# Optimization experiments

Measured on AMD Instinct MI355X. Metric: run time of the kernel, lower is better.

Reference implementation:

```python
import jax, jax.numpy as jnp
import numpy as np

HEAD_DIM = 256
NUM_HEADS = 8
NUM_KV_HEADS = 1
ROPE_BASE = 10000.0
NEG_INF = -1e9


def _rope_cos_sin(position_ids):
    # inv_freq: [head_dim/2]
    inv_freq = 1.0 / (ROPE_BASE ** (jnp.arange(0, HEAD_DIM, 2, dtype=jnp.float32) / HEAD_DIM))
    # freqs: [B, S, head_dim/2]
    freqs = position_ids.astype(jnp.float32)[:, :, None] * inv_freq[None, None, :]
    emb = jnp.concatenate([freqs, freqs], axis=-1)  # [B, S, head_dim]
    return jnp.cos(emb), jnp.sin(emb)


def _rotate_half(x):
    x1, x2 = x[..., : HEAD_DIM // 2], x[..., HEAD_DIM // 2 :]
    return jnp.concatenate([-x2, x1], axis=-1)


def setup_inputs() -> dict:
    key = jax.random.key(0)
    ks = jax.random.split(key, 5)
    B, S, D = 2, 2048, 2048
    hidden_states = jax.random.normal(ks[0], (B, S, D), dtype=jnp.float32)
    # additive causal mask: 0 on/below diagonal, -1e9 above
    causal = jnp.triu(jnp.full((S, S), NEG_INF, dtype=jnp.float32), k=1)
    attention_mask = jnp.broadcast_to(causal[None, None], (B, 1, S, S))
    position_ids = jnp.broadcast_to(jnp.arange(S, dtype=jnp.int64 if jax.config.jax_enable_x64 else jnp.int32)[None], (B, S))
    Wq = jax.random.normal(ks[1], (NUM_HEADS * HEAD_DIM, D), dtype=jnp.float32) * 0.02
    Wk = jax.random.normal(ks[2], (NUM_KV_HEADS * HEAD_DIM, D), dtype=jnp.float32) * 0.02
    Wv = jax.random.normal(ks[3], (NUM_KV_HEADS * HEAD_DIM, D), dtype=jnp.float32) * 0.02
    Wo = jax.random.normal(ks[4], (D, NUM_HEADS * HEAD_DIM), dtype=jnp.float32) * 0.02
    return {"hidden_states": hidden_states, "attention_mask": attention_mask,
            "position_ids": position_ids, "Wq": Wq, "Wk": Wk, "Wv": Wv, "Wo": Wo}


def reference(hidden_states, attention_mask, position_ids, Wq, Wk, Wv, Wo):
    B, S, D = hidden_states.shape
    n_rep = NUM_HEADS // NUM_KV_HEADS
    # projections (no bias)
    q = (hidden_states @ Wq.T).reshape(B, S, NUM_HEADS, HEAD_DIM).transpose(0, 2, 1, 3)
    k = (hidden_states @ Wk.T).reshape(B, S, NUM_KV_HEADS, HEAD_DIM).transpose(0, 2, 1, 3)
    v = (hidden_states @ Wv.T).reshape(B, S, NUM_KV_HEADS, HEAD_DIM).transpose(0, 2, 1, 3)
    # rotary embeddings, broadcast over heads (unsqueeze_dim=1)
    cos, sin = _rope_cos_sin(position_ids)  # [B, S, head_dim]
    cos, sin = cos[:, None], sin[:, None]
    q = q * cos + _rotate_half(q) * sin
    k = k * cos + _rotate_half(k) * sin
    # repeat_kv: expand kv heads to match query heads
    k = jnp.repeat(k, n_rep, axis=1)  # [B, H, S, Dh]
    v = jnp.repeat(v, n_rep, axis=1)
    scores = jnp.einsum('bhqd,bhkd->bhqk', q, k) / jnp.sqrt(jnp.float32(HEAD_DIM))
    scores = scores + attention_mask
    attn_weights = jax.nn.softmax(scores.astype(jnp.float32), axis=-1).astype(q.dtype)
    attn_output = jnp.einsum('bhqk,bhkd->bhqd', attn_weights, v)
    attn_output = attn_output.transpose(0, 2, 1, 3).reshape(B, S, NUM_HEADS * HEAD_DIM)
    attn_output = attn_output @ Wo.T
    return attn_output, attn_weights
```

## Files before the change

kernel.cpp:

```cpp
#include <hip/hip_runtime.h>
#include <math.h>

#define SEQ 2048
#define DM  2048
#define NH  8
#define HD  256
#define NB  2

typedef __attribute__((ext_vector_type(8))) short bf16x8;
typedef __attribute__((ext_vector_type(4))) float f32x4;

__device__ inline short f2b(float f) {
    union { float f; unsigned u; } x; x.f = f;
    unsigned r = x.u + 0x7fffu + ((x.u >> 16) & 1u);
    return (short)(r >> 16);
}
__device__ inline float b2f(short s) {
    union { unsigned u; float f; } x;
    x.u = ((unsigned)(unsigned short)s) << 16;
    return x.f;
}

typedef unsigned int u32_g __attribute__((address_space(1)));
typedef unsigned int u32_l __attribute__((address_space(3)));
__device__ inline void gl2lds(const void* g, void* l) {
    __builtin_amdgcn_global_load_lds((const u32_g*)g, (u32_l*)l, 16, 0, 0);
}

__global__ void convert_all(const float* __restrict__ hs, const float* __restrict__ wq,
                            const float* __restrict__ wk, const float* __restrict__ wv,
                            const float* __restrict__ wo,
                            short* __restrict__ hsb, short* __restrict__ wcat,
                            short* __restrict__ wob)
{
    int i4 = blockIdx.x * 256 + threadIdx.x;
    const float* src; short* dst; int s4, d4;
    if (i4 < 2097152)      { src = hs; dst = hsb;  s4 = i4;           d4 = s4; }
    else if (i4 < 3145728) { src = wq; dst = wcat; s4 = i4 - 2097152; d4 = s4; }
    else if (i4 < 3276800) { src = wk; dst = wcat; s4 = i4 - 3145728; d4 = 1048576 + s4; }
    else if (i4 < 3407872) { src = wv; dst = wcat; s4 = i4 - 3276800; d4 = 1179648 + s4; }
    else                   { src = wo; dst = wob;  s4 = i4 - 3407872; d4 = s4; }
    float4 v = ((const float4*)src)[s4];
    short4 o;
    o.x = f2b(v.x); o.y = f2b(v.y); o.z = f2b(v.z); o.w = f2b(v.w);
    ((short4*)dst)[d4] = o;
}

template<int MODE>
__global__ __launch_bounds__(256, 2) void gemm_bt(const short* __restrict__ A,
                                                  const short* __restrict__ Bw,
                                                  float* __restrict__ C,
                                                  short* __restrict__ q_o,
                                                  short* __restrict__ k_o,
                                                  short* __restrict__ v_o,
                                                  int M, int N, int K)
{
    __shared__ short As[128 * 32];
    __shared__ short Bs[128 * 32];
    int tid = threadIdx.x;
    int lane = tid & 63, w = tid >> 6;
    int lm = lane & 15, quad = lane >> 4;
    int wm = w & 1, wn = w >> 1;
    int m0 = blockIdx.y * 128, n0 = blockIdx.x * 128;

    f32x4 acc[16];
#pragma unroll
    for (int i = 0; i < 16; ++i) acc[i] = (f32x4){0.f, 0.f, 0.f, 0.f};

    const char* Aptr = (const char*)A + (size_t)m0 * K * 2;
    const char* Bptr = (const char*)Bw + (size_t)n0 * K * 2;

    for (int k0 = 0; k0 < K; k0 += 32) {
#pragma unroll
        for (int it = 0; it < 2; ++it) {
            int f = it * 4096 + tid * 16;
            int row = f >> 6, colb = f & 63;
            gl2lds(Aptr + (size_t)row * (K * 2) + k0 * 2 + colb, (char*)As + f);
            gl2lds(Bptr + (size_t)row * (K * 2) + k0 * 2 + colb, (char*)Bs + f);
        }
        __syncthreads();
        bf16x8 af[4], bfr[4];
#pragma unroll
        for (int mt = 0; mt < 4; ++mt)
            af[mt] = *(const bf16x8*)(As + (wm * 64 + mt * 16 + lm) * 32 + quad * 8);
#pragma unroll
        for (int nt = 0; nt < 4; ++nt)
            bfr[nt] = *(const bf16x8*)(Bs + (wn * 64 + nt * 16 + lm) * 32 + quad * 8);
#pragma unroll
        for (int mt = 0; mt < 4; ++mt)
#pragma unroll
            for (int nt = 0; nt < 4; ++nt)
                acc[mt * 4 + nt] = __builtin_amdgcn_mfma_f32_16x16x32_bf16(
                    af[mt], bfr[nt], acc[mt * 4 + nt], 0, 0, 0);
        __syncthreads();
    }

#pragma unroll
    for (int mt = 0; mt < 4; ++mt)
#pragma unroll
        for (int nt = 0; nt < 4; ++nt) {
            f32x4 a = acc[mt * 4 + nt];
            int col = n0 + wn * 64 + nt * 16 + lm;
#pragma unroll
            for (int i = 0; i < 4; ++i) {
                int m = m0 + wm * 64 + mt * 16 + quad * 4 + i;
                if (MODE == 0) {
                    C[(size_t)m * N + col] = a[i];
                } else {
                    int b = m >> 11, s = m & (SEQ - 1);
                    short hv = f2b(a[i]);
                    if (col < DM) {
                        int hh = col >> 8, d = col & (HD - 1);
                        q_o[(((size_t)(b * NH + hh)) * SEQ + s) * HD + d] = hv;
                    } else if (col < DM + HD) {
                        int d = col - DM;
                        int c2 = (d >> 3) ^ (s & 31);
                        k_o[((size_t)b * SEQ + s) * HD + (c2 << 3) + (d & 7)] = hv;
                    } else {
                        int d = col - DM - HD;
                        int sc = ((s >> 3) & 7) ^ (d & 7);
                        v_o[((size_t)(b * HD + d)) * SEQ + (s & ~63) + (sc << 3) + (s & 7)] = hv;
                    }
                }
            }
        }
}

__global__ void rope_kernel(short* __restrict__ q, short* __restrict__ k,
                            const int* __restrict__ pos)
{
    const int QP = NB * NH * SEQ * 128;
    const int KP = NB * SEQ * 128;
    const float C0 = 0.07195578415606394f;
    int idx = blockIdx.x * 256 + threadIdx.x;
    if (idx < QP) {
        int d = idx & 127;
        int s = (idx >> 7) & (SEQ - 1);
        int h = (idx >> 18) & (NH - 1);
        int b = idx >> 21;
        float p = (float)pos[b * SEQ + s];
        float fr = p * expf(-(float)d * C0);
        float c = cosf(fr), sn = sinf(fr);
        size_t base = (((size_t)(b * NH + h)) * SEQ + s) * HD + d;
        float x0 = b2f(q[base]), x1 = b2f(q[base + 128]);
        q[base]       = f2b(x0 * c - x1 * sn);
        q[base + 128] = f2b(x1 * c + x0 * sn);
    } else {
        int j = idx - QP;
        if (j < KP) {
            int d = j & 127;
            int s = (j >> 7) & (SEQ - 1);
            int b = j >> 18;
            float p = (float)pos[b * SEQ + s];
            float fr = p * expf(-(float)d * C0);
            float c = cosf(fr), sn = sinf(fr);
            int e0 = ((((d >> 3) ^ (s & 31)) & 31) << 3) | (d & 7);
            size_t base = ((size_t)(b * SEQ + s)) * HD;
            float x0 = b2f(k[base + e0]), x1 = b2f(k[base + (e0 ^ 128)]);
            k[base + e0]         = f2b(x0 * c - x1 * sn);
            k[base + (e0 ^ 128)] = f2b(x1 * c + x0 * sn);
        }
    }
}

__global__ __launch_bounds__(256, 2) void attn_flash(const short* __restrict__ qb,
                                                     const short* __restrict__ kb,
                                                     const short* __restrict__ vT,
                                                     float* __restrict__ w_out,
                                                     short* __restrict__ a_o)
{
    __shared__ short Ks[64 * 256];
    __shared__ short Vs[256 * 64];
    __shared__ short P[4][16][72];

    int tid = threadIdx.x;
    int w = tid >> 6, lane = tid & 63;
    int lm = lane & 15, quad = lane >> 4;
    int idx = blockIdx.x;
    int hb = idx & 15;
    int h = hb & 7, b = hb >> 3;
    int tq = 31 - (idx >> 4);
    int q0 = tq * 64;
    int r0 = q0 + w * 16;

    const short* qrow = qb + (((size_t)(b * NH + h)) * SEQ + r0 + lm) * HD;
    bf16x8 qf[8];
#pragma unroll
    for (int ks = 0; ks < 8; ++ks)
        qf[ks] = *(const bf16x8*)(qrow + ks * 32 + quad * 8);

    float m_r[4], l_r[4];
    f32x4 O[16];
#pragma unroll
    for (int i = 0; i < 4; ++i) { m_r[i] = -INFINITY; l_r[i] = 0.f; }
#pragma unroll
    for (int i = 0; i < 16; ++i) O[i] = (f32x4){0.f, 0.f, 0.f, 0.f};

    const short* kb0 = kb + (size_t)b * SEQ * HD;
    const short* vb0 = vT + (size_t)b * HD * SEQ;

    for (int tk = 0; tk <= tq; ++tk) {
        const char* kt = (const char*)(kb0 + (size_t)tk * 64 * HD);
#pragma unroll
        for (int it = 0; it < 8; ++it) {
            int g = it * 256 + tid;
            gl2lds(kt + ((size_t)(g >> 5) * HD + (g & 31) * 8) * 2, (char*)Ks + g * 16);
            gl2lds((const char*)vb0 + ((size_t)(g >> 3) * SEQ + tk * 64 + (g & 7) * 8) * 2,
                   (char*)Vs + g * 16);
        }
        __syncthreads();

        f32x4 sa[4];
#pragma unroll
        for (int nt = 0; nt < 4; ++nt) sa[nt] = (f32x4){0.f, 0.f, 0.f, 0.f};
#pragma unroll
        for (int ks = 0; ks < 8; ++ks)
#pragma unroll
            for (int nt = 0; nt < 4; ++nt) {
                int s_l = nt * 16 + lm;
                bf16x8 kf = *(const bf16x8*)(Ks + s_l * 256 +
                                             (((ks * 4 + quad) ^ (s_l & 31)) << 3));
                sa[nt] = __builtin_amdgcn_mfma_f32_16x16x32_bf16(qf[ks], kf, sa[nt], 0, 0, 0);
            }

        float vals[4][4];
#pragma unroll
        for (int nt = 0; nt < 4; ++nt)
#pragma unroll
            for (int i = 0; i < 4; ++i) {
                float v = sa[nt][i] * 0.0625f;
                if (tk == tq && (nt * 16 + lm) > (w * 16 + quad * 4 + i)) v -= 1e9f;
                vals[nt][i] = v;
            }
        float mnew[4], alpha[4], ps[4];
#pragma unroll
        for (int i = 0; i < 4; ++i) {
            float mx = fmaxf(fmaxf(vals[0][i], vals[1][i]), fmaxf(vals[2][i], vals[3][i]));
            mx = fmaxf(mx, __shfl_xor(mx, 1));
            mx = fmaxf(mx, __shfl_xor(mx, 2));
            mx = fmaxf(mx, __shfl_xor(mx, 4));
            mx = fmaxf(mx, __shfl_xor(mx, 8));
            mnew[i] = fmaxf(m_r[i], mx);
            alpha[i] = expf(m_r[i] - mnew[i]);
            ps[i] = 0.f;
        }
#pragma unroll
        for (int nt = 0; nt < 4; ++nt)
#pragma unroll
            for (int i = 0; i < 4; ++i) {
                float p = expf(vals[nt][i] - mnew[i]);
                ps[i] += p;
                P[w][quad * 4 + i][nt * 16 + lm] = f2b(p);
            }
        f32x4 al;
#pragma unroll
        for (int i = 0; i < 4; ++i) {
            float t = ps[i];
            t += __shfl_xor(t, 1); t += __shfl_xor(t, 2);
            t += __shfl_xor(t, 4); t += __shfl_xor(t, 8);
            l_r[i] = l_r[i] * alpha[i] + t;
            m_r[i] = mnew[i];
            al[i] = alpha[i];
        }
#pragma unroll
        for (int nt2 = 0; nt2 < 16; ++nt2) O[nt2] *= al;

        const short* prow = &P[w][lm][0];
#pragma unroll
        for (int kc = 0; kc < 2; ++kc) {
            bf16x8 pf = *(const bf16x8*)(prow + kc * 32 + quad * 8);
#pragma unroll
            for (int nt2 = 0; nt2 < 16; ++nt2) {
                int d_l = nt2 * 16 + lm;
                bf16x8 vf = *(const bf16x8*)(Vs + d_l * 64 +
                                             (((kc * 4 + quad) ^ (d_l & 7)) << 3));
                O[nt2] = __builtin_amdgcn_mfma_f32_16x16x32_bf16(pf, vf, O[nt2], 0, 0, 0);
            }
        }
        __syncthreads();
    }

    f32x4 li;
#pragma unroll
    for (int i = 0; i < 4; ++i) li[i] = 1.f / l_r[i];

#pragma unroll
    for (int nt2 = 0; nt2 < 16; ++nt2)
#pragma unroll
        for (int i = 0; i < 4; ++i) {
            size_t s = (size_t)q0 + w * 16 + quad * 4 + i;
            a_o[((size_t)b * SEQ + s) * DM + h * HD + nt2 * 16 + lm] = f2b(O[nt2][i] * li[i]);
        }

    float* wb = w_out + (((size_t)(b * NH + h)) * SEQ) * SEQ;
    for (int tk = 0; tk <= tq; ++tk) {
        const char* kt = (const char*)(kb0 + (size_t)tk * 64 * HD);
#pragma unroll
        for (int it = 0; it < 8; ++it) {
            int g = it * 256 + tid;
            gl2lds(kt + ((size_t)(g >> 5) * HD + (g & 31) * 8) * 2, (char*)Ks + g * 16);
        }
        __syncthreads();
        f32x4 sa[4];
#pragma unroll
        for (int nt = 0; nt < 4; ++nt) sa[nt] = (f32x4){0.f, 0.f, 0.f, 0.f};
#pragma unroll
        for (int ks = 0; ks < 8; ++ks)
#pragma unroll
            for (int nt = 0; nt < 4; ++nt) {
                int s_l = nt * 16 + lm;
                bf16x8 kf = *(const bf16x8*)(Ks + s_l * 256 +
                                             (((ks * 4 + quad) ^ (s_l & 31)) << 3));
                sa[nt] = __builtin_amdgcn_mfma_f32_16x16x32_bf16(qf[ks], kf, sa[nt], 0, 0, 0);
            }
#pragma unroll
        for (int nt = 0; nt < 4; ++nt)
#pragma unroll
            for (int i = 0; i < 4; ++i) {
                float v = sa[nt][i] * 0.0625f;
                if (tk == tq && (nt * 16 + lm) > (w * 16 + quad * 4 + i)) v -= 1e9f;
                float wv = expf(v - m_r[i]) * li[i];
                wb[(size_t)(r0 + quad * 4 + i) * SEQ + tk * 64 + nt * 16 + lm] = wv;
            }
        __syncthreads();
    }

    int zs = (tq + 1) * 64;
    if (zs < SEQ) {
        int r = tid >> 2, c0 = (tid & 3) * 4;
        float* wr = wb + (size_t)(q0 + r) * SEQ;
        float4 z = make_float4(0.f, 0.f, 0.f, 0.f);
        for (int c = zs + c0; c < SEQ; c += 16)
            *(float4*)(wr + c) = z;
    }
}

extern "C" void kernel_launch(void* const* d_in, const int* in_sizes, int n_in,
                              void* d_out, int out_size, void* d_ws, size_t ws_size,
                              hipStream_t stream)
{
    const float* hs   = (const float*)d_in[0];
    const int*   pos  = (const int*)d_in[2];
    const float* Wq   = (const float*)d_in[3];
    const float* Wk   = (const float*)d_in[4];
    const float* Wv   = (const float*)d_in[5];
    const float* Wo   = (const float*)d_in[6];

    float* out      = (float*)d_out;
    float* attn_out = out;
    float* w_out    = out + (size_t)NB * SEQ * DM;

    short* hsb  = (short*)d_ws;
    short* a_b  = hsb;
    short* wcat = hsb + 8388608;
    short* wob  = wcat + 5242880;
    short* qx   = wob + 4194304;
    short* kx   = qx + 8388608;
    short* vTx  = kx + 1048576;

    convert_all<<<17408, 256, 0, stream>>>(hs, Wq, Wk, Wv, Wo, hsb, wcat, wob);
    gemm_bt<1><<<dim3(20, 32), 256, 0, stream>>>(hsb, wcat, nullptr, qx, kx, vTx,
                                                 NB * SEQ, DM + 2 * HD, DM);
    rope_kernel<<<18432, 256, 0, stream>>>(qx, kx, pos);
    attn_flash<<<512, 256, 0, stream>>>(qx, kx, vTx, w_out, a_b);
    gemm_bt<0><<<dim3(16, 32), 256, 0, stream>>>(a_b, wob, attn_out, nullptr, nullptr, nullptr,
                                                 NB * SEQ, DM, DM);
}
```

Baseline: 650.9 us.

## Register-prefetch K/V tiles, fast math exp/trig, nontemporal stores, zigzag tile order

The attention kernel now prefetches the next K/V tile into registers while the current tile is computed, replacing direct global-to-LDS loads with a register-staged double buffer. It also raises wave priority around the MFMA loops, switches expf and sincos to hardware approximations (with explicit range reduction for RoPE), writes the attention weights with nontemporal stores, and alternates the query-tile order between long and short tiles across blocks for load balance. The register staging adds register pressure and may lower occupancy, and the fast math functions lose some accuracy.

```diff
diff --git a/kernel.cpp b/kernel.cpp
--- a/kernel.cpp
+++ b/kernel.cpp
@@ -132,6 +132,7 @@
     const int QP = NB * NH * SEQ * 128;
     const int KP = NB * SEQ * 128;
     const float C0 = 0.07195578415606394f;
+    const float R2PI = 0.15915494309189535f;
     int idx = blockIdx.x * 256 + threadIdx.x;
     if (idx < QP) {
         int d = idx & 127;
@@ -139,8 +140,9 @@
         int h = (idx >> 18) & (NH - 1);
         int b = idx >> 21;
         float p = (float)pos[b * SEQ + s];
-        float fr = p * expf(-(float)d * C0);
-        float c = cosf(fr), sn = sinf(fr);
+        float fr = p * __expf(-(float)d * C0);
+        float rv = fr * R2PI; rv -= floorf(rv);
+        float c = __builtin_amdgcn_cosf(rv), sn = __builtin_amdgcn_sinf(rv);
         size_t base = (((size_t)(b * NH + h)) * SEQ + s) * HD + d;
         float x0 = b2f(q[base]), x1 = b2f(q[base + 128]);
         q[base]       = f2b(x0 * c - x1 * sn);
@@ -152,8 +154,9 @@
             int s = (j >> 7) & (SEQ - 1);
             int b = j >> 18;
             float p = (float)pos[b * SEQ + s];
-            float fr = p * expf(-(float)d * C0);
-            float c = cosf(fr), sn = sinf(fr);
+            float fr = p * __expf(-(float)d * C0);
+            float rv = fr * R2PI; rv -= floorf(rv);
+            float c = __builtin_amdgcn_cosf(rv), sn = __builtin_amdgcn_sinf(rv);
             int e0 = ((((d >> 3) ^ (s & 31)) & 31) << 3) | (d & 7);
             size_t base = ((size_t)(b * SEQ + s)) * HD;
             float x0 = b2f(k[base + e0]), x1 = b2f(k[base + (e0 ^ 128)]);
@@ -179,7 +182,7 @@
     int idx = blockIdx.x;
     int hb = idx & 15;
     int h = hb & 7, b = hb >> 3;
-    int tq = 31 - (idx >> 4);
+    int tq = (idx < 256) ? (31 - (idx >> 4)) : ((idx - 256) >> 4);
     int q0 = tq * 64;
     int r0 = q0 + w * 16;
 
@@ -199,20 +202,43 @@
     const short* kb0 = kb + (size_t)b * SEQ * HD;
     const short* vb0 = vT + (size_t)b * HD * SEQ;
 
-    for (int tk = 0; tk <= tq; ++tk) {
-        const char* kt = (const char*)(kb0 + (size_t)tk * 64 * HD);
+    f32x4 kreg[8], vreg[8];
+
+    auto issue_kv = [&](int t) {
+        const short* kt = kb0 + (size_t)t * 64 * HD;
+        const short* vt = vb0 + (size_t)t * 64;
 #pragma unroll
         for (int it = 0; it < 8; ++it) {
             int g = it * 256 + tid;
-            gl2lds(kt + ((size_t)(g >> 5) * HD + (g & 31) * 8) * 2, (char*)Ks + g * 16);
-            gl2lds((const char*)vb0 + ((size_t)(g >> 3) * SEQ + tk * 64 + (g & 7) * 8) * 2,
-                   (char*)Vs + g * 16);
-        }
-        __syncthreads();
+            kreg[it] = *(const f32x4*)(kt + (g >> 5) * HD + (g & 31) * 8);
+            vreg[it] = *(const f32x4*)(vt + (size_t)(g >> 3) * SEQ + (g & 7) * 8);
+        }
+    };
+    auto issue_k = [&](int t) {
+        const short* kt = kb0 + (size_t)t * 64 * HD;
+#pragma unroll
+        for (int it = 0; it < 8; ++it) {
+            int g = it * 256 + tid;
+            kreg[it] = *(const f32x4*)(kt + (g >> 5) * HD + (g & 31) * 8);
+        }
+    };
+
+    issue_kv(0);
+
+    for (int tk = 0; tk <= tq; ++tk) {
+#pragma unroll
+        for (int it = 0; it < 8; ++it) {
+            int g = it * 256 + tid;
+            *(f32x4*)((char*)Ks + g * 16) = kreg[it];
+            *(f32x4*)((char*)Vs + g * 16) = vreg[it];
+        }
+        __syncthreads();
+        if (tk < tq) issue_kv(tk + 1);
 
         f32x4 sa[4];
 #pragma unroll
         for (int nt = 0; nt < 4; ++nt) sa[nt] = (f32x4){0.f, 0.f, 0.f, 0.f};
+        __builtin_amdgcn_s_setprio(1);
 #pragma unroll
         for (int ks = 0; ks < 8; ++ks)
 #pragma unroll
@@ -222,6 +248,7 @@
                                              (((ks * 4 + quad) ^ (s_l & 31)) << 3));
                 sa[nt] = __builtin_amdgcn_mfma_f32_16x16x32_bf16(qf[ks], kf, sa[nt], 0, 0, 0);
             }
+        __builtin_amdgcn_s_setprio(0);
 
         float vals[4][4];
 #pragma unroll
@@ -241,14 +268,14 @@
             mx = fmaxf(mx, __shfl_xor(mx, 4));
             mx = fmaxf(mx, __shfl_xor(mx, 8));
             mnew[i] = fmaxf(m_r[i], mx);
-            alpha[i] = expf(m_r[i] - mnew[i]);
+            alpha[i] = __expf(m_r[i] - mnew[i]);
             ps[i] = 0.f;
         }
 #pragma unroll
         for (int nt = 0; nt < 4; ++nt)
 #pragma unroll
             for (int i = 0; i < 4; ++i) {
-                float p = expf(vals[nt][i] - mnew[i]);
+                float p = __expf(vals[nt][i] - mnew[i]);
                 ps[i] += p;
                 P[w][quad * 4 + i][nt * 16 + lm] = f2b(p);
             }
@@ -266,6 +293,7 @@
         for (int nt2 = 0; nt2 < 16; ++nt2) O[nt2] *= al;
 
         const short* prow = &P[w][lm][0];
+        __builtin_amdgcn_s_setprio(1);
 #pragma unroll
         for (int kc = 0; kc < 2; ++kc) {
             bf16x8 pf = *(const bf16x8*)(prow + kc * 32 + quad * 8);
@@ -277,12 +305,15 @@
                 O[nt2] = __builtin_amdgcn_mfma_f32_16x16x32_bf16(pf, vf, O[nt2], 0, 0, 0);
             }
         }
+        __builtin_amdgcn_s_setprio(0);
         __syncthreads();
     }
 
     f32x4 li;
 #pragma unroll
     for (int i = 0; i < 4; ++i) li[i] = 1.f / l_r[i];
+
+    issue_k(0);
 
 #pragma unroll
     for (int nt2 = 0; nt2 < 16; ++nt2)
@@ -294,16 +325,18 @@
 
     float* wb = w_out + (((size_t)(b * NH + h)) * SEQ) * SEQ;
     for (int tk = 0; tk <= tq; ++tk) {
-        const char* kt = (const char*)(kb0 + (size_t)tk * 64 * HD);
 #pragma unroll
         for (int it = 0; it < 8; ++it) {
             int g = it * 256 + tid;
-            gl2lds(kt + ((size_t)(g >> 5) * HD + (g & 31) * 8) * 2, (char*)Ks + g * 16);
-        }
-        __syncthreads();
+            *(f32x4*)((char*)Ks + g * 16) = kreg[it];
+        }
+        __syncthreads();
+        if (tk < tq) issue_k(tk + 1);
+
         f32x4 sa[4];
 #pragma unroll
         for (int nt = 0; nt < 4; ++nt) sa[nt] = (f32x4){0.f, 0.f, 0.f, 0.f};
+        __builtin_amdgcn_s_setprio(1);
 #pragma unroll
         for (int ks = 0; ks < 8; ++ks)
 #pragma unroll
@@ -313,14 +346,16 @@
                                              (((ks * 4 + quad) ^ (s_l & 31)) << 3));
                 sa[nt] = __builtin_amdgcn_mfma_f32_16x16x32_bf16(qf[ks], kf, sa[nt], 0, 0, 0);
             }
+        __builtin_amdgcn_s_setprio(0);
 #pragma unroll
         for (int nt = 0; nt < 4; ++nt)
 #pragma unroll
             for (int i = 0; i < 4; ++i) {
                 float v = sa[nt][i] * 0.0625f;
                 if (tk == tq && (nt * 16 + lm) > (w * 16 + quad * 4 + i)) v -= 1e9f;
-                float wv = expf(v - m_r[i]) * li[i];
-                wb[(size_t)(r0 + quad * 4 + i) * SEQ + tk * 64 + nt * 16 + lm] = wv;
+                float wv = __expf(v - m_r[i]) * li[i];
+                __builtin_nontemporal_store(
+                    wv, wb + (size_t)(r0 + quad * 4 + i) * SEQ + tk * 64 + nt * 16 + lm);
             }
         __syncthreads();
     }
@@ -329,9 +364,9 @@
     if (zs < SEQ) {
         int r = tid >> 2, c0 = (tid & 3) * 4;
         float* wr = wb + (size_t)(q0 + r) * SEQ;
-        float4 z = make_float4(0.f, 0.f, 0.f, 0.f);
+        f32x4 z = (f32x4){0.f, 0.f, 0.f, 0.f};
         for (int c = zs + c0; c < SEQ; c += 16)
-            *(float4*)(wr + c) = z;
+            __builtin_nontemporal_store(z, (f32x4*)(wr + c));
     }
 }
 
```

New measurement: 622.7 us. 4.3% less time.
